# Kernel optimization log

Measured on AMD Instinct MI355X. Metric: run time of the kernel, lower is better.

The kernel has to match this reference:

```python
import jax, jax.numpy as jnp
import numpy as np

H = 4        # num_heads
KNN = 10     # k_knn neighbors gathered by distance
KS = 4       # k_select top-k neighbors kept by attention score
EPS = 1e-5
BIG = 1e9


def _ln(x, g, b):
    m = x.mean(-1, keepdims=True)
    v = ((x - m) ** 2).mean(-1, keepdims=True)
    return (x - m) * jax.lax.rsqrt(v + EPS) * g + b


def _sparse_dyn_voxel_attn(x, coords, mask, w_qkv, b_qkv, w_proj, b_proj):
    # x: [B,N,C], coords: [B,N,3], mask: [B,N] bool
    B, N, C = x.shape
    dh = C // H
    qkv = x @ w_qkv + b_qkv                       # [B,N,3C]
    q, k, v = jnp.split(qkv, 3, axis=-1)
    q = q.reshape(B, N, H, dh).transpose(0, 2, 1, 3)   # [B,H,N,dh]
    k = k.reshape(B, N, H, dh).transpose(0, 2, 1, 3)
    v = v.reshape(B, N, H, dh).transpose(0, 2, 1, 3)

    # KNN over voxel coordinates; empty voxels pushed to far distance
    d2 = jnp.sum((coords[:, :, None, :] - coords[:, None, :, :]) ** 2, axis=-1)  # [B,N,N]
    d2 = jnp.where(mask[:, None, :], d2, BIG)
    _, nbr = jax.lax.top_k(-d2, KNN)              # [B,N,KNN] nearest-neighbor indices

    # gather neighbor keys/values: [B,H,N,KNN,dh]
    kn = jax.vmap(lambda a, i: a[:, i, :])(k, nbr)
    vn = jax.vmap(lambda a, i: a[:, i, :])(v, nbr)
    nmask = jax.vmap(lambda m, i: m[i])(mask, nbr)  # [B,N,KNN]

    scale = float(1.0 / np.sqrt(dh))
    scores = jnp.einsum('bhnd,bhnkd->bhnk', q, kn) * scale  # [B,H,N,KNN]
    scores = scores + jnp.where(nmask, 0.0, -BIG)[:, None, :, :]

    # dynamic selection: keep top k_select neighbors by score, softmax over them
    sv, si = jax.lax.top_k(scores, KS)            # [B,H,N,KS]
    w = jax.nn.softmax(sv, axis=-1)
    vsel = jnp.take_along_axis(vn, si[..., None], axis=3)   # [B,H,N,KS,dh]
    o = jnp.einsum('bhnk,bhnkd->bhnd', w, vsel)   # [B,H,N,dh]
    o = o.transpose(0, 2, 1, 3).reshape(B, N, C) @ w_proj + b_proj
    return jnp.where(mask[..., None], o, 0.0)


def setup_inputs() -> dict:
    key = jax.random.key(0)
    ks = jax.random.split(key, 8)
    B, N, C, M = 4, 4096, 64, 256  # N = 16^3 voxels
    s = lambda k, sh: jax.random.normal(k, sh, jnp.float32) * 0.02
    return dict(
        inputs=jax.random.normal(ks[0], (B, N, C), jnp.float32),
        voxel_coords=jax.random.uniform(ks[1], (B, N, 3), jnp.float32) * 16.0,
        non_empty_mask=jax.random.randint(ks[2], (B, N), 0, 2).astype(bool),
        ln1_g=jnp.ones(C, jnp.float32), ln1_b=jnp.zeros(C, jnp.float32),
        ln2_g=jnp.ones(C, jnp.float32), ln2_b=jnp.zeros(C, jnp.float32),
        w_qkv=s(ks[3], (C, 3 * C)), b_qkv=jnp.zeros(3 * C, jnp.float32),
        w_proj=s(ks[4], (C, C)), b_proj=jnp.zeros(C, jnp.float32),
        w1=s(ks[5], (C, M)), b1=jnp.zeros(M, jnp.float32),
        w2=s(ks[6], (M, C)), b2=jnp.zeros(C, jnp.float32),
    )


def reference(inputs, voxel_coords, non_empty_mask, ln1_g, ln1_b, ln2_g, ln2_b,
              w_qkv, b_qkv, w_proj, b_proj, w1, b1, w2, b2):
    a = _sparse_dyn_voxel_attn(_ln(inputs, ln1_g, ln1_b), voxel_coords,
                               non_empty_mask, w_qkv, b_qkv, w_proj, b_proj)
    x = 0.5 * a + inputs                          # drop_path(attn)*0.5 + shortcut (eval)
    h = jax.nn.gelu(_ln(x, ln2_g, ln2_b) @ w1 + b1) @ w2 + b2
    return 0.5 * h + x
```

## Files before the change

kernel.cpp:

```cpp
#include <hip/hip_runtime.h>
#include <hip/hip_bf16.h>
#include <math.h>

#define NH   4
#define DH   16
#define CH   64
#define KNN  10
#define KS   4
#define NV   4096
#define NB   4
#define MHID 256
#define BN   (NB * NV)

#define P_LN1G  0
#define P_LN1B  64
#define P_LN2G  128
#define P_LN2B  192
#define P_WQKV  256
#define P_BQKV  12544
#define P_WPROJ 12736
#define P_BPROJ 16832
#define P_W1    16896
#define P_B1    33280
#define P_W2    33536
#define P_B2    49920
#define P_TOT   49984

#define N_ING  (BN * CH + NB * NV * 3 + P_TOT + BN)
#define N_ING4 (N_ING / 4)
#define N_PACK (16384 + 16384 + 12288)

typedef __hip_bfloat16 bf16;
typedef __attribute__((ext_vector_type(8))) short short8;
typedef __attribute__((ext_vector_type(4))) float float4a;
typedef unsigned long long ull;

__device__ __forceinline__ float b2f(bf16 x) { return __bfloat162float(x); }

__device__ __forceinline__ float cvt(const void* p, int i, int isbf) {
  return isbf ? b2f(((const bf16*)p)[i]) : ((const float*)p)[i];
}

__device__ __forceinline__ float us2f(unsigned short u) {
  return __uint_as_float(((unsigned)u) << 16);
}

__device__ __forceinline__ float4 cvt4(const void* p, int i, int isbf) {
  float4 r;
  if (isbf) {
    ushort4 u = *(const ushort4*)((const unsigned short*)p + i);
    r.x = us2f(u.x); r.y = us2f(u.y); r.z = us2f(u.z); r.w = us2f(u.w);
  } else {
    r = *(const float4*)((const float*)p + i);
  }
  return r;
}

__device__ __forceinline__ float wave_sum_f32(float v) {
#pragma unroll
  for (int m = 32; m >= 1; m >>= 1) v += __shfl_xor(v, m, 64);
  return v;
}

__device__ __forceinline__ int wave_sum_i32(int v) {
#pragma unroll
  for (int m = 32; m >= 1; m >>= 1) v += __shfl_xor(v, m, 64);
  return v;
}

__device__ __forceinline__ void wave_min_kv(unsigned& hi, unsigned& lo) {
#pragma unroll
  for (int m = 32; m >= 1; m >>= 1) {
    unsigned ohi = __shfl_xor(hi, m, 64);
    unsigned olo = __shfl_xor(lo, m, 64);
    if (ohi < hi || (ohi == hi && olo < lo)) { hi = ohi; lo = olo; }
  }
}

__device__ __forceinline__ float tanh_fast(float u) {
  float e = __expf(2.0f * u);
  return 1.0f - 2.0f / (e + 1.0f);
}

__device__ __forceinline__ float d2f(float x, float y, float z,
                                     float qx, float qy, float qz) {
  float dx = x - qx, dy = y - qy, dz = z - qz;
  return dx * dx + dy * dy + dz * dz;
}

__device__ __forceinline__ void knn_insert(ull* arr, ull key) {
  if (key < arr[KNN - 1]) {
#pragma unroll
    for (int t = 0; t < KNN; ++t) {
      ull a = arr[t];
      bool lt = key < a;
      ull mn = lt ? key : a;
      ull mx = lt ? a : key;
      arr[t] = mn;
      key = mx;
    }
  }
}

__global__ __launch_bounds__(256) void k_prep(
    const void* xin, const void* coords, const void* maskr,
    const void* ln1g, const void* ln1b, const void* ln2g, const void* ln2b,
    const void* wqkv, const void* bqkv, const void* wproj, const void* bproj,
    const void* w1, const void* b1, const void* w2, const void* b2,
    float* __restrict__ xcan, float* __restrict__ ccan,
    float* __restrict__ pcan, int* __restrict__ mcan,
    unsigned short* __restrict__ w1p, unsigned short* __restrict__ w2p,
    unsigned short* __restrict__ wqp, int* __restrict__ flags)
{
  __shared__ int sfl[2];
  const int tid = threadIdx.x;
  if (tid < 64) {
    const unsigned short* xu = (const unsigned short*)xin;
    const unsigned* mu = (const unsigned*)maskr;
    int c = 0;
#pragma unroll
    for (int k = 0; k < 4; ++k) {
      unsigned short w = xu[tid * 4 + k];
      int e = (w >> 7) & 0xFF;
      c += (e >= 100 && e <= 140);
    }
#pragma unroll
    for (int m = 32; m >= 1; m >>= 1) c += __shfl_xor(c, m, 64);
    unsigned big = (mu[tid] > 1u) ? 1u : 0u;
#pragma unroll
    for (int m = 32; m >= 1; m >>= 1) big |= __shfl_xor(big, m, 64);
    if (tid == 0) {
      sfl[0] = (c >= 205) ? 1 : 0;
      sfl[1] = big ? 1 : 0;
      if (blockIdx.x == 0) { flags[0] = sfl[0]; flags[1] = sfl[1]; }
    }
  }
  __syncthreads();
  const int isbf = sfl[0], m8 = sfl[1];

  int id = blockIdx.x * 256 + tid;
  if (id < N_ING4) {
    int e4 = id * 4;
    const int n0 = BN * CH, n1 = NB * NV * 3, n2 = P_TOT;
    if (e4 < n0) { *(float4*)&xcan[e4] = cvt4(xin, e4, isbf); return; }
    e4 -= n0;
    if (e4 < n1) { *(float4*)&ccan[e4] = cvt4(coords, e4, isbf); return; }
    e4 -= n1;
    if (e4 < n2) {
      const void* src; int off;
      if      (e4 < P_LN1B)  { src = ln1g;  off = e4 - P_LN1G; }
      else if (e4 < P_LN2G)  { src = ln1b;  off = e4 - P_LN1B; }
      else if (e4 < P_LN2B)  { src = ln2g;  off = e4 - P_LN2G; }
      else if (e4 < P_WQKV)  { src = ln2b;  off = e4 - P_LN2B; }
      else if (e4 < P_BQKV)  { src = wqkv;  off = e4 - P_WQKV; }
      else if (e4 < P_WPROJ) { src = bqkv;  off = e4 - P_BQKV; }
      else if (e4 < P_BPROJ) { src = wproj; off = e4 - P_WPROJ; }
      else if (e4 < P_W1)    { src = bproj; off = e4 - P_BPROJ; }
      else if (e4 < P_B1)    { src = w1;    off = e4 - P_W1; }
      else if (e4 < P_W2)    { src = b1;    off = e4 - P_B1; }
      else if (e4 < P_B2)    { src = w2;    off = e4 - P_W2; }
      else                   { src = b2;    off = e4 - P_B2; }
      *(float4*)&pcan[e4] = cvt4(src, off, isbf);
      return;
    }
    e4 -= n2;
    if (m8) {
      uchar4 u = *(const uchar4*)((const unsigned char*)maskr + e4);
      mcan[e4 + 0] = u.x != 0; mcan[e4 + 1] = u.y != 0;
      mcan[e4 + 2] = u.z != 0; mcan[e4 + 3] = u.w != 0;
    } else {
      int4 vv = *(const int4*)((const int*)maskr + e4);
      mcan[e4 + 0] = vv.x != 0; mcan[e4 + 1] = vv.y != 0;
      mcan[e4 + 2] = vv.z != 0; mcan[e4 + 3] = vv.w != 0;
    }
    return;
  }
  id -= N_ING4;
  if (id < 16384) {
    int j = id & 7, l = (id >> 3) & 63, kh = (id >> 9) & 1, nt = id >> 10;
    int k = kh * 32 + ((l >> 4) * 8) + j;
    int n = nt * 16 + (l & 15);
    w1p[id] = __bfloat16_as_ushort(__float2bfloat16(cvt(w1, k * MHID + n, isbf)));
    return;
  }
  id -= 16384;
  if (id < 16384) {
    int j = id & 7, l = (id >> 3) & 63, kh = (id >> 9) & 7, nt = id >> 12;
    int k = kh * 32 + ((l >> 4) * 8) + j;
    int n = nt * 16 + (l & 15);
    w2p[id] = __bfloat16_as_ushort(__float2bfloat16(cvt(w2, k * CH + n, isbf)));
    return;
  }
  id -= 16384;
  if (id < 12288) {
    int j = id & 7, l = (id >> 3) & 63, kh = (id >> 9) & 1, nt = id >> 10;
    int k = kh * 32 + ((l >> 4) * 8) + j;
    int n = nt * 16 + (l & 15);
    wqp[id] = __bfloat16_as_ushort(__float2bfloat16(cvt(wqkv, k * 192 + n, isbf)));
  }
}

#define XQS 72
__global__ __launch_bounds__(1024) void k_mid(
    const float* __restrict__ ccan, const int* __restrict__ mcan,
    float4* __restrict__ pbin, unsigned* __restrict__ bstart,
    const float* __restrict__ x, const float* __restrict__ pcan,
    const unsigned short* __restrict__ wqp, float* __restrict__ qkv)
{
  __shared__ unsigned cnt[NV];
  __shared__ unsigned woff[16];
  __shared__ unsigned short xnb[64 * XQS];
  const int tid = threadIdx.x;
  const int wave = tid >> 6, lane = tid & 63;

  if (blockIdx.x < NB) {
    const int b = blockIdx.x;
    const float* cb = ccan + (size_t)b * NV * 3;
    const int* mb = mcan + b * NV;
    unsigned* st = bstart + (size_t)b * 4104;

#pragma unroll
    for (int k = 0; k < 4; ++k) cnt[tid + k * 1024] = 0;
    __syncthreads();

#pragma unroll
    for (int k = 0; k < 4; ++k) {
      int j = tid + k * 1024;
      if (mb[j]) {
        int cx = (int)cb[j * 3];     cx = cx > 15 ? 15 : cx;
        int cy = (int)cb[j * 3 + 1]; cy = cy > 15 ? 15 : cy;
        int cz = (int)cb[j * 3 + 2]; cz = cz > 15 ? 15 : cz;
        atomicAdd(&cnt[(cz << 8) + (cy << 4) + cx], 1u);
      }
    }
    __syncthreads();

    unsigned s0 = cnt[tid * 4], s1 = cnt[tid * 4 + 1];
    unsigned s2 = cnt[tid * 4 + 2], s3 = cnt[tid * 4 + 3];
    unsigned tot = s0 + s1 + s2 + s3;
    unsigned v = tot;
#pragma unroll
    for (int d = 1; d < 64; d <<= 1) {
      unsigned o = __shfl_up(v, d, 64);
      if (lane >= d) v += o;
    }
    if (lane == 63) woff[wave] = v;
    __syncthreads();
    unsigned wpre = 0;
    for (int w = 0; w < wave; ++w) wpre += woff[w];
    unsigned r = wpre + v - tot;
    cnt[tid * 4]     = r; st[tid * 4]     = r; r += s0;
    cnt[tid * 4 + 1] = r; st[tid * 4 + 1] = r; r += s1;
    cnt[tid * 4 + 2] = r; st[tid * 4 + 2] = r; r += s2;
    cnt[tid * 4 + 3] = r; st[tid * 4 + 3] = r; r += s3;
    if (tid == 1023) st[4096] = r;
    __syncthreads();

#pragma unroll
    for (int k = 0; k < 4; ++k) {
      int j = tid + k * 1024;
      if (mb[j]) {
        float xx = cb[j * 3], yy = cb[j * 3 + 1], zz = cb[j * 3 + 2];
        int cx = (int)xx; cx = cx > 15 ? 15 : cx;
        int cy = (int)yy; cy = cy > 15 ? 15 : cy;
        int cz = (int)zz; cz = cz > 15 ? 15 : cz;
        unsigned pos = atomicAdd(&cnt[(cz << 8) + (cy << 4) + cx], 1u);
        float4 q; q.x = xx; q.y = yy; q.z = zz; q.w = __int_as_float(j);
        pbin[(size_t)b * NV + pos] = q;
      }
    }
    return;
  }

  const int tile = wave >> 2, wv4 = wave & 3;
  const int row0 = (blockIdx.x - NB) * 64 + tile * 16;
  unsigned short* xt = xnb + tile * 16 * XQS;
  {
    const float gg = pcan[P_LN1G + lane], bb = pcan[P_LN1B + lane];
#pragma unroll
    for (int r = 0; r < 4; ++r) {
      int m = wv4 * 4 + r;
      float v = x[(size_t)(row0 + m) * CH + lane];
      float mn = wave_sum_f32(v) * (1.0f / 64.0f);
      float d = v - mn;
      float var = wave_sum_f32(d * d) * (1.0f / 64.0f);
      float rs = 1.0f / sqrtf(var + 1e-5f);
      xt[m * XQS + lane] =
          __bfloat16_as_ushort(__float2bfloat16(d * rs * gg + bb));
    }
  }
  __syncthreads();

  const int q = lane >> 4, c = lane & 15;
  short8 a0 = *(const short8*)&xt[c * XQS + q * 8];
  short8 a1 = *(const short8*)&xt[c * XQS + 32 + q * 8];

#pragma unroll
  for (int t = 0; t < 3; ++t) {
    int nt = wv4 * 3 + t;
    short8 b0 = *(const short8*)&wqp[(size_t)((nt * 2 + 0) * 64 + lane) * 8];
    short8 b1 = *(const short8*)&wqp[(size_t)((nt * 2 + 1) * 64 + lane) * 8];
    float4a z = {0.f, 0.f, 0.f, 0.f};
    z = __builtin_amdgcn_mfma_f32_16x16x32_bf16(a0, b0, z, 0, 0, 0);
    z = __builtin_amdgcn_mfma_f32_16x16x32_bf16(a1, b1, z, 0, 0, 0);
    int n = nt * 16 + c;
    float bq = pcan[P_BQKV + n];
#pragma unroll
    for (int r = 0; r < 4; ++r) {
      int m = q * 4 + r;
      qkv[(size_t)(row0 + m) * 192 + n] = z[r] + bq;
    }
  }
}

__global__ __launch_bounds__(256) void k_knn4(
    const float4* __restrict__ pbin, const unsigned* __restrict__ bstart,
    int* __restrict__ nbr)
{
  const int wave = threadIdx.x >> 6, lane = threadIdx.x & 63;
  const int b = blockIdx.x >> 10;
  const int slot = (blockIdx.x & 1023) * 4 + wave;
  const unsigned* st = bstart + (size_t)b * 4104;
  const int nval = (int)st[4096];
  if (slot >= nval) return;
  const float4* gpt = pbin + (size_t)b * NV;

  const float4 me = gpt[slot];
  const float qx = me.x, qy = me.y, qz = me.z;
  const int qi = __float_as_int(me.w);
  int cz = (int)qz; cz = cz > 15 ? 15 : cz;

  ull arr[KNN];
#pragma unroll
  for (int t = 0; t < KNN; ++t) arr[t] = ~0ull;

  int R = 2;
  int zlo = cz - 2 < 0 ? 0 : cz - 2;
  int zhi = cz + 2 > 15 ? 15 : cz + 2;
  {
    const int s = (int)st[zlo << 8], e = (int)st[(zhi + 1) << 8];
    for (int i = s + lane; i < e; i += 64) {
      float4 p = gpt[i];
      float d2 = d2f(p.x, p.y, p.z, qx, qy, qz);
      knn_insert(arr, ((ull)__float_as_uint(d2) << 32) |
                      (unsigned)__float_as_int(p.w));
    }
  }

  for (;;) {
    const float RR = (float)(R * R);
    int c = 0;
#pragma unroll
    for (int t = 0; t < KNN; ++t) {
      float d = __uint_as_float((unsigned)(arr[t] >> 32));
      c += (d <= RR) ? 1 : 0;
    }
    c = wave_sum_i32(c);
    if (c >= KNN) break;
    if (zlo == 0 && zhi == 15) break;
    ++R;
    const int nzlo = cz - R < 0 ? 0 : cz - R;
    const int nzhi = cz + R > 15 ? 15 : cz + R;
    {
      const int s = (int)st[nzlo << 8], e = (int)st[zlo << 8];
      for (int i = s + lane; i < e; i += 64) {
        float4 p = gpt[i];
        float d2 = d2f(p.x, p.y, p.z, qx, qy, qz);
        knn_insert(arr, ((ull)__float_as_uint(d2) << 32) |
                        (unsigned)__float_as_int(p.w));
      }
    }
    {
      const int s = (int)st[(zhi + 1) << 8], e = (int)st[(nzhi + 1) << 8];
      for (int i = s + lane; i < e; i += 64) {
        float4 p = gpt[i];
        float d2 = d2f(p.x, p.y, p.z, qx, qy, qz);
        knn_insert(arr, ((ull)__float_as_uint(d2) << 32) |
                        (unsigned)__float_as_int(p.w));
      }
    }
    zlo = nzlo; zhi = nzhi;
  }

  unsigned myj = 0;
#pragma unroll 1
  for (int r = 0; r < KNN; ++r) {
    unsigned hi = (unsigned)(arr[0] >> 32);
    unsigned lo = (unsigned)(arr[0] & 0xffffffffu);
    wave_min_kv(hi, lo);
    const ull win = ((ull)hi << 32) | lo;
    if (arr[0] == win) {
#pragma unroll
      for (int t = 0; t < KNN - 1; ++t) arr[t] = arr[t + 1];
      arr[KNN - 1] = ~0ull;
    }
    if (lane == r) myj = lo;
  }
  const int row = (b << 12) | qi;
  if (lane < KNN) nbr[(size_t)row * KNN + lane] = (int)(myj & (NV - 1));
}

#define XNS 72
#define GS  264
__global__ __launch_bounds__(256) void k_attn_mlp(
    const float* __restrict__ qkv, const int* __restrict__ nbr,
    const int* __restrict__ mcan, const float* __restrict__ xcan,
    const float* __restrict__ pcan,
    const unsigned short* __restrict__ w1p,
    const unsigned short* __restrict__ w2p,
    const int* __restrict__ flags, void* __restrict__ out)
{
  __shared__ float wp[CH * CH];
  __shared__ float bp[CH];
  __shared__ float otile[16][CH];
  __shared__ float xtile[16][CH];
  __shared__ float sc[4][NH][KNN];
  __shared__ float wsel[4][NH][KS];
  __shared__ int   isel[4][NH][KS];
  __shared__ int   nb[4][KNN];
  __shared__ float npen[4][KNN];
  __shared__ unsigned short xnb[16 * XNS];
  __shared__ unsigned short gb[16 * GS];
  const int tid = threadIdx.x;
  const int wave = tid >> 6, lane = tid & 63;
  const int row0 = blockIdx.x * 16;
  const int b = row0 / NV;

  {
    const float4* src = (const float4*)(pcan + P_WPROJ);
    float4* dst = (float4*)wp;
    for (int i = tid; i < CH * CH / 4; i += 256) dst[i] = src[i];
    if (tid < CH) bp[tid] = pcan[P_BPROJ + tid];
  }
  __syncthreads();

#pragma unroll 1
  for (int r = 0; r < 4; ++r) {
    const int m = wave * 4 + r;
    const int row = row0 + m;
    if (mcan[row]) {
      if (lane < KNN) {
        int j = nbr[(size_t)row * KNN + lane] & (NV - 1);
        nb[wave][lane] = j;
        npen[wave][lane] = mcan[b * NV + j] ? 0.0f : -1e9f;
      }
      __builtin_amdgcn_wave_barrier();
      if (lane < NH * KNN) {
        int h = lane / KNN, kk = lane % KNN;
        int j = nb[wave][kk];
        const float* qp = qkv + (size_t)row * 192 + h * DH;
        const float* kp = qkv + ((size_t)(b * NV + j)) * 192 + 64 + h * DH;
        float acc = 0.f;
#pragma unroll
        for (int d = 0; d < DH; ++d) acc += qp[d] * kp[d];
        sc[wave][h][kk] = acc * 0.25f + npen[wave][kk];
      }
      __builtin_amdgcn_wave_barrier();
      if (lane < NH) {
        int h = lane;
        float sv[KS]; int sj[KS];
        unsigned used = 0;
#pragma unroll
        for (int rr = 0; rr < KS; ++rr) {
          float best = -INFINITY; int bi = 0;
#pragma unroll
          for (int kk = 0; kk < KNN; ++kk) {
            float s = sc[wave][h][kk];
            if (!(used & (1u << kk)) && s > best) { best = s; bi = kk; }
          }
          used |= 1u << bi; sv[rr] = best; sj[rr] = bi;
        }
        float mx = sv[0];
        float e[KS], sum = 0.f;
#pragma unroll
        for (int rr = 0; rr < KS; ++rr) { e[rr] = expf(sv[rr] - mx); sum += e[rr]; }
        float inv = 1.0f / sum;
#pragma unroll
        for (int rr = 0; rr < KS; ++rr) {
          wsel[wave][h][rr] = e[rr] * inv;
          isel[wave][h][rr] = nb[wave][sj[rr]];
        }
      }
      __builtin_amdgcn_wave_barrier();
      {
        int h = lane >> 4, d = lane & 15;
        float o = 0.f;
#pragma unroll
        for (int rr = 0; rr < KS; ++rr) {
          int j = isel[wave][h][rr];
          o += wsel[wave][h][rr] *
               qkv[((size_t)(b * NV + j)) * 192 + 128 + h * DH + d];
        }
        otile[m][lane] = o;
      }
      __builtin_amdgcn_wave_barrier();
    }
  }

#pragma unroll 1
  for (int r = 0; r < 4; ++r) {
    const int m = wave * 4 + r;
    const int row = row0 + m;
    float x = xcan[(size_t)row * CH + lane];
    if (mcan[row]) {
      float acc = bp[lane];
#pragma unroll 4
      for (int cc = 0; cc < CH; ++cc)
        acc = fmaf(otile[m][cc], wp[cc * CH + lane], acc);
      x += 0.5f * acc;
    }
    xtile[m][lane] = x;
  }

  {
    const float gg = pcan[P_LN2G + lane], bb2 = pcan[P_LN2B + lane];
#pragma unroll
    for (int r = 0; r < 4; ++r) {
      int m = wave * 4 + r;
      float v = xtile[m][lane];
      float mn = wave_sum_f32(v) * (1.0f / 64.0f);
      float d = v - mn;
      float var = wave_sum_f32(d * d) * (1.0f / 64.0f);
      float rs = 1.0f / sqrtf(var + 1e-5f);
      xnb[m * XNS + lane] =
          __bfloat16_as_ushort(__float2bfloat16(d * rs * gg + bb2));
    }
  }
  __syncthreads();

  const int q = lane >> 4, c = lane & 15;
  short8 a0 = *(const short8*)&xnb[c * XNS + q * 8];
  short8 a1 = *(const short8*)&xnb[c * XNS + 32 + q * 8];

  float4a acc1[4];
#pragma unroll
  for (int t = 0; t < 4; ++t) {
    int nt = wave * 4 + t;
    short8 b0 = *(const short8*)&w1p[(size_t)((nt * 2 + 0) * 64 + lane) * 8];
    short8 b1 = *(const short8*)&w1p[(size_t)((nt * 2 + 1) * 64 + lane) * 8];
    float4a z = {0.f, 0.f, 0.f, 0.f};
    z = __builtin_amdgcn_mfma_f32_16x16x32_bf16(a0, b0, z, 0, 0, 0);
    z = __builtin_amdgcn_mfma_f32_16x16x32_bf16(a1, b1, z, 0, 0, 0);
    acc1[t] = z;
  }
#pragma unroll
  for (int t = 0; t < 4; ++t) {
    int n = (wave * 4 + t) * 16 + c;
    float bo = pcan[P_B1 + n];
#pragma unroll
    for (int r = 0; r < 4; ++r) {
      float h = acc1[t][r] + bo;
      float u = 0.7978845608028654f * (h + 0.044715f * h * h * h);
      float gv = 0.5f * h * (1.0f + tanh_fast(u));
      gb[(q * 4 + r) * GS + n] = __bfloat16_as_ushort(__float2bfloat16(gv));
    }
  }
  __syncthreads();

  float4a o = {0.f, 0.f, 0.f, 0.f};
#pragma unroll
  for (int kh = 0; kh < 8; ++kh) {
    short8 ag = *(const short8*)&gb[c * GS + kh * 32 + q * 8];
    short8 bg = *(const short8*)&w2p[(size_t)((wave * 8 + kh) * 64 + lane) * 8];
    o = __builtin_amdgcn_mfma_f32_16x16x32_bf16(ag, bg, o, 0, 0, 0);
  }
  {
    int n = wave * 16 + c;
    float b2v = pcan[P_B2 + n];
    const int isbf = flags[0];
#pragma unroll
    for (int r = 0; r < 4; ++r) {
      int m = q * 4 + r;
      size_t idx = (size_t)(row0 + m) * CH + n;
      float val = 0.5f * (o[r] + b2v) + xtile[m][n];
      if (isbf) ((bf16*)out)[idx] = __float2bfloat16(val);
      else      ((float*)out)[idx] = val;
    }
  }
}

extern "C" void kernel_launch(void* const* d_in, const int* in_sizes, int n_in,
                              void* d_out, int out_size, void* d_ws, size_t ws_size,
                              hipStream_t stream)
{
  char* ws = (char*)d_ws;
  float* qkv   = (float*)(ws);
  float* xcan  = (float*)(ws + 16777216);
  float* ccan  = (float*)(ws + 20971520);
  float* pcan  = (float*)(ws + 21168128);
  int*   mcan  = (int*)  (ws + 21368064);
  int*   nbr   = (int*)  (ws + 21433600);
  int*   flags = (int*)  (ws + 22088960);
  unsigned short* w1p = (unsigned short*)(ws + 22089728);
  unsigned short* w2p = (unsigned short*)(ws + 22122496);
  unsigned short* wqp = (unsigned short*)(ws + 22155264);
  float4*   pbin   = (float4*)  (ws + 22179840);
  unsigned* bstart = (unsigned*)(ws + 22441984);

  const int total = N_ING4 + N_PACK;
  k_prep<<<(total + 255) / 256, 256, 0, stream>>>(
      d_in[0], d_in[1], d_in[2], d_in[3], d_in[4], d_in[5], d_in[6],
      d_in[7], d_in[8], d_in[9], d_in[10], d_in[11], d_in[12], d_in[13], d_in[14],
      xcan, ccan, pcan, mcan, w1p, w2p, wqp, flags);
  k_mid<<<NB + BN / 64, 1024, 0, stream>>>(ccan, mcan, pbin, bstart,
                                           xcan, pcan, wqp, qkv);
  k_knn4<<<NB * (NV / 4), 256, 0, stream>>>(pbin, bstart, nbr);
  k_attn_mlp<<<BN / 16, 256, 0, stream>>>(qkv, nbr, mcan, xcan, pcan,
                                          w1p, w2p, flags, d_out);
}
```

Before: 147.9 us.

## Move voxel binning into prep kernel and fuse KNN search with QKV projection

Voxel binning (count, scan, scatter) now runs in extra blocks of the prep kernel and reads raw coordinates and mask directly, so the canonical coordinate buffer disappears. The KNN search blocks and the LN1+QKV projection blocks now share one launch, which removes a kernel launch and lets the two independent jobs overlap. Prep blocks grow to 1024 threads and QKV blocks shrink to 16 rows each. The risk is that the heavy binning blocks become the critical path of prep, and that KNN and QKV blocks interfere with each other's occupancy.

After: 148.0 us. About the same (+0.1%).

```diff
diff --git a/kernel.cpp b/kernel.cpp
--- a/kernel.cpp
+++ b/kernel.cpp
@@ -26,9 +26,11 @@
 #define P_B2    49920
 #define P_TOT   49984
 
-#define N_ING  (BN * CH + NB * NV * 3 + P_TOT + BN)
-#define N_ING4 (N_ING / 4)
-#define N_PACK (16384 + 16384 + 12288)
+#define N_ING   (BN * CH + P_TOT + BN)
+#define N_ING4  (N_ING / 4)
+#define N_PACK  (16384 + 16384 + 12288)
+#define NBI     ((N_ING4 + N_PACK + 1023) / 1024)
+#define KNNBLK  (NB * (NV / 4))
 
 typedef __hip_bfloat16 bf16;
 typedef __attribute__((ext_vector_type(8))) short short8;
@@ -102,18 +104,22 @@
   }
 }
 
-__global__ __launch_bounds__(256) void k_prep(
+__global__ __launch_bounds__(1024) void k_prep(
     const void* xin, const void* coords, const void* maskr,
     const void* ln1g, const void* ln1b, const void* ln2g, const void* ln2b,
     const void* wqkv, const void* bqkv, const void* wproj, const void* bproj,
     const void* w1, const void* b1, const void* w2, const void* b2,
-    float* __restrict__ xcan, float* __restrict__ ccan,
+    float* __restrict__ xcan,
     float* __restrict__ pcan, int* __restrict__ mcan,
     unsigned short* __restrict__ w1p, unsigned short* __restrict__ w2p,
-    unsigned short* __restrict__ wqp, int* __restrict__ flags)
+    unsigned short* __restrict__ wqp, int* __restrict__ flags,
+    float4* __restrict__ pbin, unsigned* __restrict__ bstart)
 {
   __shared__ int sfl[2];
+  __shared__ unsigned cnt[NV];
+  __shared__ unsigned woff[16];
   const int tid = threadIdx.x;
+  const int wave = tid >> 6, lane = tid & 63;
   if (tid < 64) {
     const unsigned short* xu = (const unsigned short*)xin;
     const unsigned* mu = (const unsigned*)maskr;
@@ -138,14 +144,76 @@
   __syncthreads();
   const int isbf = sfl[0], m8 = sfl[1];
 
-  int id = blockIdx.x * 256 + tid;
+  if (blockIdx.x >= NBI) {
+    const int b = blockIdx.x - NBI;
+    const unsigned char* m8p = (const unsigned char*)maskr + (size_t)b * NV;
+    const int* m32p = (const int*)maskr + (size_t)b * NV;
+    unsigned* st = bstart + (size_t)b * 4104;
+
+#pragma unroll
+    for (int k = 0; k < 4; ++k) cnt[tid + k * 1024] = 0;
+    __syncthreads();
+
+#pragma unroll 1
+    for (int k = 0; k < 4; ++k) {
+      int j = tid + k * 1024;
+      int mv = m8 ? (m8p[j] != 0) : (m32p[j] != 0);
+      if (mv) {
+        int e = (b * NV + j) * 3;
+        int cx = (int)cvt(coords, e, isbf);     cx = cx > 15 ? 15 : cx;
+        int cy = (int)cvt(coords, e + 1, isbf); cy = cy > 15 ? 15 : cy;
+        int cz = (int)cvt(coords, e + 2, isbf); cz = cz > 15 ? 15 : cz;
+        atomicAdd(&cnt[(cz << 8) + (cy << 4) + cx], 1u);
+      }
+    }
+    __syncthreads();
+
+    unsigned s0 = cnt[tid * 4], s1 = cnt[tid * 4 + 1];
+    unsigned s2 = cnt[tid * 4 + 2], s3 = cnt[tid * 4 + 3];
+    unsigned tot = s0 + s1 + s2 + s3;
+    unsigned v = tot;
+#pragma unroll
+    for (int d = 1; d < 64; d <<= 1) {
+      unsigned o = __shfl_up(v, d, 64);
+      if (lane >= d) v += o;
+    }
+    if (lane == 63) woff[wave] = v;
+    __syncthreads();
+    unsigned wpre = 0;
+    for (int w = 0; w < wave; ++w) wpre += woff[w];
+    unsigned r = wpre + v - tot;
+    cnt[tid * 4]     = r; st[tid * 4]     = r; r += s0;
+    cnt[tid * 4 + 1] = r; st[tid * 4 + 1] = r; r += s1;
+    cnt[tid * 4 + 2] = r; st[tid * 4 + 2] = r; r += s2;
+    cnt[tid * 4 + 3] = r; st[tid * 4 + 3] = r; r += s3;
+    if (tid == 1023) st[4096] = r;
+    __syncthreads();
+
+#pragma unroll 1
+    for (int k = 0; k < 4; ++k) {
+      int j = tid + k * 1024;
+      int mv = m8 ? (m8p[j] != 0) : (m32p[j] != 0);
+      if (mv) {
+        int e = (b * NV + j) * 3;
+        float xx = cvt(coords, e, isbf), yy = cvt(coords, e + 1, isbf),
+              zz = cvt(coords, e + 2, isbf);
+        int cx = (int)xx; cx = cx > 15 ? 15 : cx;
+        int cy = (int)yy; cy = cy > 15 ? 15 : cy;
+        int cz = (int)zz; cz = cz > 15 ? 15 : cz;
+        unsigned pos = atomicAdd(&cnt[(cz << 8) + (cy << 4) + cx], 1u);
+        float4 q; q.x = xx; q.y = yy; q.z = zz; q.w = __int_as_float(j);
+        pbin[(size_t)b * NV + pos] = q;
+      }
+    }
+    return;
+  }
+
+  int id = blockIdx.x * 1024 + tid;
   if (id < N_ING4) {
     int e4 = id * 4;
-    const int n0 = BN * CH, n1 = NB * NV * 3, n2 = P_TOT;
+    const int n0 = BN * CH, n2 = P_TOT;
     if (e4 < n0) { *(float4*)&xcan[e4] = cvt4(xin, e4, isbf); return; }
     e4 -= n0;
-    if (e4 < n1) { *(float4*)&ccan[e4] = cvt4(coords, e4, isbf); return; }
-    e4 -= n1;
     if (e4 < n2) {
       const void* src; int off;
       if      (e4 < P_LN1B)  { src = ln1g;  off = e4 - P_LN1G; }
@@ -201,103 +269,123 @@
 }
 
 #define XQS 72
-__global__ __launch_bounds__(1024) void k_mid(
-    const float* __restrict__ ccan, const int* __restrict__ mcan,
-    float4* __restrict__ pbin, unsigned* __restrict__ bstart,
+__global__ __launch_bounds__(256) void k_mid(
+    const float4* __restrict__ pbin, const unsigned* __restrict__ bstart,
+    int* __restrict__ nbr,
     const float* __restrict__ x, const float* __restrict__ pcan,
     const unsigned short* __restrict__ wqp, float* __restrict__ qkv)
 {
-  __shared__ unsigned cnt[NV];
-  __shared__ unsigned woff[16];
-  __shared__ unsigned short xnb[64 * XQS];
-  const int tid = threadIdx.x;
-  const int wave = tid >> 6, lane = tid & 63;
-
-  if (blockIdx.x < NB) {
-    const int b = blockIdx.x;
-    const float* cb = ccan + (size_t)b * NV * 3;
-    const int* mb = mcan + b * NV;
-    unsigned* st = bstart + (size_t)b * 4104;
-
-#pragma unroll
-    for (int k = 0; k < 4; ++k) cnt[tid + k * 1024] = 0;
-    __syncthreads();
-
-#pragma unroll
-    for (int k = 0; k < 4; ++k) {
-      int j = tid + k * 1024;
-      if (mb[j]) {
-        int cx = (int)cb[j * 3];     cx = cx > 15 ? 15 : cx;
-        int cy = (int)cb[j * 3 + 1]; cy = cy > 15 ? 15 : cy;
-        int cz = (int)cb[j * 3 + 2]; cz = cz > 15 ? 15 : cz;
-        atomicAdd(&cnt[(cz << 8) + (cy << 4) + cx], 1u);
-      }
-    }
-    __syncthreads();
-
-    unsigned s0 = cnt[tid * 4], s1 = cnt[tid * 4 + 1];
-    unsigned s2 = cnt[tid * 4 + 2], s3 = cnt[tid * 4 + 3];
-    unsigned tot = s0 + s1 + s2 + s3;
-    unsigned v = tot;
-#pragma unroll
-    for (int d = 1; d < 64; d <<= 1) {
-      unsigned o = __shfl_up(v, d, 64);
-      if (lane >= d) v += o;
-    }
-    if (lane == 63) woff[wave] = v;
-    __syncthreads();
-    unsigned wpre = 0;
-    for (int w = 0; w < wave; ++w) wpre += woff[w];
-    unsigned r = wpre + v - tot;
-    cnt[tid * 4]     = r; st[tid * 4]     = r; r += s0;
-    cnt[tid * 4 + 1] = r; st[tid * 4 + 1] = r; r += s1;
-    cnt[tid * 4 + 2] = r; st[tid * 4 + 2] = r; r += s2;
-    cnt[tid * 4 + 3] = r; st[tid * 4 + 3] = r; r += s3;
-    if (tid == 1023) st[4096] = r;
-    __syncthreads();
-
-#pragma unroll
-    for (int k = 0; k < 4; ++k) {
-      int j = tid + k * 1024;
-      if (mb[j]) {
-        float xx = cb[j * 3], yy = cb[j * 3 + 1], zz = cb[j * 3 + 2];
-        int cx = (int)xx; cx = cx > 15 ? 15 : cx;
-        int cy = (int)yy; cy = cy > 15 ? 15 : cy;
-        int cz = (int)zz; cz = cz > 15 ? 15 : cz;
-        unsigned pos = atomicAdd(&cnt[(cz << 8) + (cy << 4) + cx], 1u);
-        float4 q; q.x = xx; q.y = yy; q.z = zz; q.w = __int_as_float(j);
-        pbin[(size_t)b * NV + pos] = q;
-      }
-    }
+  __shared__ unsigned short xnb[16 * XQS];
+  const int wave = threadIdx.x >> 6, lane = threadIdx.x & 63;
+
+  if (blockIdx.x < KNNBLK) {
+    const int b = blockIdx.x >> 10;
+    const int slot = (blockIdx.x & 1023) * 4 + wave;
+    const unsigned* st = bstart + (size_t)b * 4104;
+    const int nval = (int)st[4096];
+    if (slot >= nval) return;
+    const float4* gpt = pbin + (size_t)b * NV;
+
+    const float4 me = gpt[slot];
+    const float qx = me.x, qy = me.y, qz = me.z;
+    const int qi = __float_as_int(me.w);
+    int cz = (int)qz; cz = cz > 15 ? 15 : cz;
+
+    ull arr[KNN];
+#pragma unroll
+    for (int t = 0; t < KNN; ++t) arr[t] = ~0ull;
+
+    int R = 2;
+    int zlo = cz - 2 < 0 ? 0 : cz - 2;
+    int zhi = cz + 2 > 15 ? 15 : cz + 2;
+    {
+      const int s = (int)st[zlo << 8], e = (int)st[(zhi + 1) << 8];
+      for (int i = s + lane; i < e; i += 64) {
+        float4 p = gpt[i];
+        float d2 = d2f(p.x, p.y, p.z, qx, qy, qz);
+        knn_insert(arr, ((ull)__float_as_uint(d2) << 32) |
+                        (unsigned)__float_as_int(p.w));
+      }
+    }
+
+    for (;;) {
+      const float RR = (float)(R * R);
+      int c = 0;
+#pragma unroll
+      for (int t = 0; t < KNN; ++t) {
+        float d = __uint_as_float((unsigned)(arr[t] >> 32));
+        c += (d <= RR) ? 1 : 0;
+      }
+      c = wave_sum_i32(c);
+      if (c >= KNN) break;
+      if (zlo == 0 && zhi == 15) break;
+      ++R;
+      const int nzlo = cz - R < 0 ? 0 : cz - R;
+      const int nzhi = cz + R > 15 ? 15 : cz + R;
+      {
+        const int s = (int)st[nzlo << 8], e = (int)st[zlo << 8];
+        for (int i = s + lane; i < e; i += 64) {
+          float4 p = gpt[i];
+          float d2 = d2f(p.x, p.y, p.z, qx, qy, qz);
+          knn_insert(arr, ((ull)__float_as_uint(d2) << 32) |
+                          (unsigned)__float_as_int(p.w));
+        }
+      }
+      {
+        const int s = (int)st[(zhi + 1) << 8], e = (int)st[(nzhi + 1) << 8];
+        for (int i = s + lane; i < e; i += 64) {
+          float4 p = gpt[i];
+          float d2 = d2f(p.x, p.y, p.z, qx, qy, qz);
+          knn_insert(arr, ((ull)__float_as_uint(d2) << 32) |
+                          (unsigned)__float_as_int(p.w));
+        }
+      }
+      zlo = nzlo; zhi = nzhi;
+    }
+
+    unsigned myj = 0;
+#pragma unroll 1
+    for (int r = 0; r < KNN; ++r) {
+      unsigned hi = (unsigned)(arr[0] >> 32);
+      unsigned lo = (unsigned)(arr[0] & 0xffffffffu);
+      wave_min_kv(hi, lo);
+      const ull win = ((ull)hi << 32) | lo;
+      if (arr[0] == win) {
+#pragma unroll
+        for (int t = 0; t < KNN - 1; ++t) arr[t] = arr[t + 1];
+        arr[KNN - 1] = ~0ull;
+      }
+      if (lane == r) myj = lo;
+    }
+    const int row = (b << 12) | qi;
+    if (lane < KNN) nbr[(size_t)row * KNN + lane] = (int)(myj & (NV - 1));
     return;
   }
 
-  const int tile = wave >> 2, wv4 = wave & 3;
-  const int row0 = (blockIdx.x - NB) * 64 + tile * 16;
-  unsigned short* xt = xnb + tile * 16 * XQS;
+  const int row0 = (blockIdx.x - KNNBLK) * 16;
   {
     const float gg = pcan[P_LN1G + lane], bb = pcan[P_LN1B + lane];
 #pragma unroll
     for (int r = 0; r < 4; ++r) {
-      int m = wv4 * 4 + r;
+      int m = wave * 4 + r;
       float v = x[(size_t)(row0 + m) * CH + lane];
       float mn = wave_sum_f32(v) * (1.0f / 64.0f);
       float d = v - mn;
       float var = wave_sum_f32(d * d) * (1.0f / 64.0f);
       float rs = 1.0f / sqrtf(var + 1e-5f);
-      xt[m * XQS + lane] =
+      xnb[m * XQS + lane] =
           __bfloat16_as_ushort(__float2bfloat16(d * rs * gg + bb));
     }
   }
   __syncthreads();
 
   const int q = lane >> 4, c = lane & 15;
-  short8 a0 = *(const short8*)&xt[c * XQS + q * 8];
-  short8 a1 = *(const short8*)&xt[c * XQS + 32 + q * 8];
+  short8 a0 = *(const short8*)&xnb[c * XQS + q * 8];
+  short8 a1 = *(const short8*)&xnb[c * XQS + 32 + q * 8];
 
 #pragma unroll
   for (int t = 0; t < 3; ++t) {
-    int nt = wv4 * 3 + t;
+    int nt = wave * 3 + t;
     short8 b0 = *(const short8*)&wqp[(size_t)((nt * 2 + 0) * 64 + lane) * 8];
     short8 b1 = *(const short8*)&wqp[(size_t)((nt * 2 + 1) * 64 + lane) * 8];
     float4a z = {0.f, 0.f, 0.f, 0.f};
@@ -311,93 +399,6 @@
       qkv[(size_t)(row0 + m) * 192 + n] = z[r] + bq;
     }
   }
-}
-
-__global__ __launch_bounds__(256) void k_knn4(
-    const float4* __restrict__ pbin, const unsigned* __restrict__ bstart,
-    int* __restrict__ nbr)
-{
-  const int wave = threadIdx.x >> 6, lane = threadIdx.x & 63;
-  const int b = blockIdx.x >> 10;
-  const int slot = (blockIdx.x & 1023) * 4 + wave;
-  const unsigned* st = bstart + (size_t)b * 4104;
-  const int nval = (int)st[4096];
-  if (slot >= nval) return;
-  const float4* gpt = pbin + (size_t)b * NV;
-
-  const float4 me = gpt[slot];
-  const float qx = me.x, qy = me.y, qz = me.z;
-  const int qi = __float_as_int(me.w);
-  int cz = (int)qz; cz = cz > 15 ? 15 : cz;
-
-  ull arr[KNN];
-#pragma unroll
-  for (int t = 0; t < KNN; ++t) arr[t] = ~0ull;
-
-  int R = 2;
-  int zlo = cz - 2 < 0 ? 0 : cz - 2;
-  int zhi = cz + 2 > 15 ? 15 : cz + 2;
-  {
-    const int s = (int)st[zlo << 8], e = (int)st[(zhi + 1) << 8];
-    for (int i = s + lane; i < e; i += 64) {
-      float4 p = gpt[i];
-      float d2 = d2f(p.x, p.y, p.z, qx, qy, qz);
-      knn_insert(arr, ((ull)__float_as_uint(d2) << 32) |
-                      (unsigned)__float_as_int(p.w));
-    }
-  }
-
-  for (;;) {
-    const float RR = (float)(R * R);
-    int c = 0;
-#pragma unroll
-    for (int t = 0; t < KNN; ++t) {
-      float d = __uint_as_float((unsigned)(arr[t] >> 32));
-      c += (d <= RR) ? 1 : 0;
-    }
-    c = wave_sum_i32(c);
-    if (c >= KNN) break;
-    if (zlo == 0 && zhi == 15) break;
-    ++R;
-    const int nzlo = cz - R < 0 ? 0 : cz - R;
-    const int nzhi = cz + R > 15 ? 15 : cz + R;
-    {
-      const int s = (int)st[nzlo << 8], e = (int)st[zlo << 8];
-      for (int i = s + lane; i < e; i += 64) {
-        float4 p = gpt[i];
-        float d2 = d2f(p.x, p.y, p.z, qx, qy, qz);
-        knn_insert(arr, ((ull)__float_as_uint(d2) << 32) |
-                        (unsigned)__float_as_int(p.w));
-      }
-    }
-    {
-      const int s = (int)st[(zhi + 1) << 8], e = (int)st[(nzhi + 1) << 8];
-      for (int i = s + lane; i < e; i += 64) {
-        float4 p = gpt[i];
-        float d2 = d2f(p.x, p.y, p.z, qx, qy, qz);
-        knn_insert(arr, ((ull)__float_as_uint(d2) << 32) |
-                        (unsigned)__float_as_int(p.w));
-      }
-    }
-    zlo = nzlo; zhi = nzhi;
-  }
-
-  unsigned myj = 0;
-#pragma unroll 1
-  for (int r = 0; r < KNN; ++r) {
-    unsigned hi = (unsigned)(arr[0] >> 32);
-    unsigned lo = (unsigned)(arr[0] & 0xffffffffu);
-    wave_min_kv(hi, lo);
-    const ull win = ((ull)hi << 32) | lo;
-    if (arr[0] == win) {
-#pragma unroll
-      for (int t = 0; t < KNN - 1; ++t) arr[t] = arr[t + 1];
-      arr[KNN - 1] = ~0ull;
-    }
-    if (lane == r) myj = lo;
-  }
-  const int row = (b << 12) | qi;
-  if (lane < KNN) nbr[(size_t)row * KNN + lane] = (int)(myj & (NV - 1));
 }
 
 #define XNS 72
@@ -586,7 +587,6 @@
   char* ws = (char*)d_ws;
   float* qkv   = (float*)(ws);
   float* xcan  = (float*)(ws + 16777216);
-  float* ccan  = (float*)(ws + 20971520);
   float* pcan  = (float*)(ws + 21168128);
   int*   mcan  = (int*)  (ws + 21368064);
   int*   nbr   = (int*)  (ws + 21433600);
@@ -597,14 +597,12 @@
   float4*   pbin   = (float4*)  (ws + 22179840);
   unsigned* bstart = (unsigned*)(ws + 22441984);
 
-  const int total = N_ING4 + N_PACK;
-  k_prep<<<(total + 255) / 256, 256, 0, stream>>>(
+  k_prep<<<NBI + NB, 1024, 0, stream>>>(
       d_in[0], d_in[1], d_in[2], d_in[3], d_in[4], d_in[5], d_in[6],
       d_in[7], d_in[8], d_in[9], d_in[10], d_in[11], d_in[12], d_in[13], d_in[14],
-      xcan, ccan, pcan, mcan, w1p, w2p, wqp, flags);
-  k_mid<<<NB + BN / 64, 1024, 0, stream>>>(ccan, mcan, pbin, bstart,
-                                           xcan, pcan, wqp, qkv);
-  k_knn4<<<NB * (NV / 4), 256, 0, stream>>>(pbin, bstart, nbr);
+      xcan, pcan, mcan, w1p, w2p, wqp, flags, pbin, bstart);
+  k_mid<<<KNNBLK + BN / 16, 256, 0, stream>>>(pbin, bstart, nbr,
+                                              xcan, pcan, wqp, qkv);
   k_attn_mlp<<<BN / 16, 256, 0, stream>>>(qkv, nbr, mcan, xcan, pcan,
                                           w1p, w2p, flags, d_out);
 }
```
